# Kernel tuning notes

Measured on AMD Instinct MI355X. Metric: run time of the kernel, lower is better.

## Reference

```python
import jax, jax.numpy as jnp
import numpy as np

N = 2048      # factor dims (d_in == units == N)
K = 16        # nonzeros per row of each factor
B = 16384     # batch
F = 3         # number of sparse factors
NNZ = N * K


def _pattern(f):
    # Fixed, compile-time-known structured sparsity pattern (butterfly-like):
    # row r has nonzeros at cols (r + k*(N//K) + f) % N, k in [0, K)
    r = np.repeat(np.arange(N), K)
    k = np.tile(np.arange(K), N)
    c = (r + k * (N // K) + f) % N
    return r.astype(np.int32), c.astype(np.int32)


def setup_inputs() -> dict:
    key = jax.random.key(0)
    kx, k0, k1, k2, ks, kb = jax.random.split(key, 6)
    # glorot-ish scale for sparse factor values: fan ~ K nonzeros per row
    wscale = (2.0 / (K + K)) ** 0.5
    rows0, cols0 = _pattern(0)
    rows1, cols1 = _pattern(1)
    rows2, cols2 = _pattern(2)
    return {
        "x": jax.random.normal(kx, (B, N), dtype=jnp.float32),
        "vals0": jax.random.normal(k0, (NNZ,), dtype=jnp.float32) * wscale,
        "vals1": jax.random.normal(k1, (NNZ,), dtype=jnp.float32) * wscale,
        "vals2": jax.random.normal(k2, (NNZ,), dtype=jnp.float32) * wscale,
        "rows0": jnp.asarray(rows0), "cols0": jnp.asarray(cols0),
        "rows1": jnp.asarray(rows1), "cols1": jnp.asarray(cols1),
        "rows2": jnp.asarray(rows2), "cols2": jnp.asarray(cols2),
        "scaling": jax.random.uniform(ks, (1,), dtype=jnp.float32, minval=0.5, maxval=1.5),
        "bias": jax.random.normal(kb, (N,), dtype=jnp.float32) * 0.02,
    }


def _dense_factor(vals, rows, cols):
    # materialize the sparse factor (values scattered into the fixed pattern)
    return jnp.zeros((N, N), dtype=vals.dtype).at[rows, cols].set(vals)


def reference(x, vals0, vals1, vals2, rows0, cols0, rows1, cols1, rows2, cols2, scaling, bias):
    # output = relu(scaling * (x @ W0 @ W1 @ W2) + bias)
    y = x
    for vals, rows, cols in ((vals0, rows0, cols0), (vals1, rows1, cols1), (vals2, rows2, cols2)):
        y = y @ _dense_factor(vals, rows, cols)  # [B, N]
    y = scaling * y + bias
    return jax.nn.relu(y)
```

## Files before the change

### kernel.cpp

```cpp
#include <hip/hip_runtime.h>

#define NN 2048
#define KK 16

__global__ __launch_bounds__(256) void sfd_compose01(const float* __restrict__ v0,
                                                     const float* __restrict__ v1,
                                                     float* __restrict__ w01) {
  int tid = blockIdx.x * 256 + threadIdx.x;
  int c1 = tid >> 4;
  int i  = tid & 15;
  int cm = (c1 + NN - 1) & (NN - 1);
  int s1 = cm & 127;
  int t1 = cm >> 7;
  int rx = s1 + (i << 7);
  float acc = 0.f;
#pragma unroll
  for (int k1 = 0; k1 < 16; ++k1) {
    int r0 = (cm - (k1 << 7)) & (NN - 1);
    int k0 = (t1 - k1 - i) & 15;
    acc = fmaf(v1[r0 * 16 + k1], v0[rx * 16 + k0], acc);
  }
  w01[c1 * 16 + i] = acc;
}

__global__ __launch_bounds__(256) void sfd_compose012(const float* __restrict__ v2,
                                                      const float* __restrict__ w01,
                                                      const float* __restrict__ scaling,
                                                      float* __restrict__ mcl) {
  int tid = blockIdx.x * 256 + threadIdx.x;
  int c = tid >> 4;
  int i = tid & 15;
  float acc = 0.f;
#pragma unroll
  for (int k2 = 0; k2 < 16; ++k2) {
    int r1 = (c + NN - 2 - (k2 << 7)) & (NN - 1);
    acc = fmaf(v2[r1 * 16 + k2], w01[r1 * 16 + i], acc);
  }
  int s = c & 127;
  int j = c >> 7;
  mcl[(s * 16 + j) * 16 + i] = acc * scaling[0];
}

__global__ __launch_bounds__(256) void sfd_apply(const float* __restrict__ x,
                                                 const float* __restrict__ mcl,
                                                 const float* __restrict__ bias,
                                                 float* __restrict__ out) {
  const int S0 = blockIdx.x << 5;
  const int b0 = blockIdx.y << 6;
  const int t = threadIdx.x;
  const int s_idx = t & 31;
  const int jp = t >> 5;
  const int s = S0 + s_idx;
  const int j0 = jp << 1;

  float mc0[16], mc1[16];
  {
    const float4* p0 = (const float4*)(mcl + ((s * 16 + j0) << 4));
    const float4* p1 = (const float4*)(mcl + ((s * 16 + j0 + 1) << 4));
#pragma unroll
    for (int q = 0; q < 4; ++q) {
      float4 a = p0[q];
      mc0[4 * q + 0] = a.x; mc0[4 * q + 1] = a.y;
      mc0[4 * q + 2] = a.z; mc0[4 * q + 3] = a.w;
      float4 b = p1[q];
      mc1[4 * q + 0] = b.x; mc1[4 * q + 1] = b.y;
      mc1[4 * q + 2] = b.z; mc1[4 * q + 3] = b.w;
    }
  }
  const int c0 = s + (j0 << 7);
  const int c1 = c0 + 128;
  const float bi0 = bias[c0];
  const float bi1 = bias[c1];

  __shared__ float xs[8 * 512];

  for (int ch = 0; ch < 8; ++ch) {
    const int rb = b0 + (ch << 3);
#pragma unroll
    for (int q = 0; q < 16; ++q) {
      int idx = t + (q << 8);
      int u = idx & 31;
      int i = (idx >> 5) & 15;
      int r = idx >> 9;
      int col = ((S0 + 125 + u) & 127) + (i << 7);
      xs[idx] = x[(size_t)(rb + r) * NN + col];
    }
    __syncthreads();
#pragma unroll 1
    for (int r = 0; r < 8; ++r) {
      const float* xr = xs + (r << 9) + s_idx;
      float acc0 = 0.f, acc1 = 0.f;
#pragma unroll
      for (int i = 0; i < 16; ++i) {
        float xv = xr[i << 5];
        acc0 = fmaf(xv, mc0[i], acc0);
        acc1 = fmaf(xv, mc1[i], acc1);
      }
      size_t ob = (size_t)(rb + r) * NN;
      out[ob + c0] = fmaxf(acc0 + bi0, 0.f);
      out[ob + c1] = fmaxf(acc1 + bi1, 0.f);
    }
    __syncthreads();
  }
}

extern "C" void kernel_launch(void* const* d_in, const int* in_sizes, int n_in,
                              void* d_out, int out_size, void* d_ws, size_t ws_size,
                              hipStream_t stream) {
  const float* x       = (const float*)d_in[0];
  const float* v0      = (const float*)d_in[1];
  const float* v1      = (const float*)d_in[2];
  const float* v2      = (const float*)d_in[3];
  const float* scaling = (const float*)d_in[10];
  const float* bias    = (const float*)d_in[11];
  float* out = (float*)d_out;

  float* w01 = (float*)d_ws;
  float* mcl = w01 + NN * KK;

  const int B = in_sizes[0] / NN;

  hipLaunchKernelGGL(sfd_compose01, dim3(128), dim3(256), 0, stream, v0, v1, w01);
  hipLaunchKernelGGL(sfd_compose012, dim3(128), dim3(256), 0, stream, v2, w01, scaling, mcl);
  hipLaunchKernelGGL(sfd_apply, dim3(4, B >> 6), dim3(256), 0, stream, x, mcl, bias, out);
}
```

Baseline: 272.5 us.

## Re-layout shared x tile for float4 reads, halve batch per block, nontemporal stores

The apply kernel's shared-memory tile changes from an i-major layout to a per-(row,u) layout padded to 20 floats, so each thread reads its 16 x values with four float4 loads. To keep the math correct, the coefficients are rotated per thread by a wraparound shift. Each block now covers 32 batch rows instead of 64, which doubles the grid, and the launch bound requests 8 blocks per CU. Bias is folded into the accumulator init and outputs use nontemporal stores to avoid cache pollution. The cost is scalar global loads for coefficients and x gathers.

```diff
diff --git a/kernel.cpp b/kernel.cpp
--- a/kernel.cpp
+++ b/kernel.cpp
@@ -41,30 +41,28 @@
   mcl[(s * 16 + j) * 16 + i] = acc * scaling[0];
 }
 
-__global__ __launch_bounds__(256) void sfd_apply(const float* __restrict__ x,
-                                                 const float* __restrict__ mcl,
-                                                 const float* __restrict__ bias,
-                                                 float* __restrict__ out) {
+__global__ __launch_bounds__(256, 8) void sfd_apply(const float* __restrict__ x,
+                                                    const float* __restrict__ mcl,
+                                                    const float* __restrict__ bias,
+                                                    float* __restrict__ out) {
   const int S0 = blockIdx.x << 5;
-  const int b0 = blockIdx.y << 6;
+  const int b0 = blockIdx.y << 5;
   const int t = threadIdx.x;
-  const int s_idx = t & 31;
+  const int u = t & 31;
   const int jp = t >> 5;
-  const int s = S0 + s_idx;
+  const int s = S0 + u;
   const int j0 = jp << 1;
+  const int w0 = (S0 + 125) & 127;
+  const int shift = (w0 + u) >> 7;
 
   float mc0[16], mc1[16];
   {
-    const float4* p0 = (const float4*)(mcl + ((s * 16 + j0) << 4));
-    const float4* p1 = (const float4*)(mcl + ((s * 16 + j0 + 1) << 4));
+    const float* r0p = mcl + ((s * 16 + j0) << 4);
 #pragma unroll
-    for (int q = 0; q < 4; ++q) {
-      float4 a = p0[q];
-      mc0[4 * q + 0] = a.x; mc0[4 * q + 1] = a.y;
-      mc0[4 * q + 2] = a.z; mc0[4 * q + 3] = a.w;
-      float4 b = p1[q];
-      mc1[4 * q + 0] = b.x; mc1[4 * q + 1] = b.y;
-      mc1[4 * q + 2] = b.z; mc1[4 * q + 3] = b.w;
+    for (int i = 0; i < 16; ++i) {
+      int ic = (i + shift) & 15;
+      mc0[i] = r0p[ic];
+      mc1[i] = r0p[16 + ic];
     }
   }
   const int c0 = s + (j0 << 7);
@@ -72,33 +70,43 @@
   const float bi0 = bias[c0];
   const float bi1 = bias[c1];
 
-  __shared__ float xs[8 * 512];
+  __shared__ float xs[8 * 32 * 20];
 
-  for (int ch = 0; ch < 8; ++ch) {
+  for (int ch = 0; ch < 4; ++ch) {
     const int rb = b0 + (ch << 3);
 #pragma unroll
-    for (int q = 0; q < 16; ++q) {
+    for (int q = 0; q < 4; ++q) {
       int idx = t + (q << 8);
-      int u = idx & 31;
-      int i = (idx >> 5) & 15;
-      int r = idx >> 9;
-      int col = ((S0 + 125 + u) & 127) + (i << 7);
-      xs[idx] = x[(size_t)(rb + r) * NN + col];
+      int uu = idx & 31;
+      int ig = (idx >> 5) & 3;
+      int rr = idx >> 7;
+      const float* xrow = x + (size_t)(rb + rr) * NN;
+      int cb = w0 + uu + (ig << 9);
+      float4 v;
+      v.x = xrow[cb & (NN - 1)];
+      v.y = xrow[(cb + 128) & (NN - 1)];
+      v.z = xrow[(cb + 256) & (NN - 1)];
+      v.w = xrow[(cb + 384) & (NN - 1)];
+      *(float4*)(xs + (rr * 32 + uu) * 20 + (ig << 2)) = v;
     }
     __syncthreads();
 #pragma unroll 1
     for (int r = 0; r < 8; ++r) {
-      const float* xr = xs + (r << 9) + s_idx;
-      float acc0 = 0.f, acc1 = 0.f;
+      const float4* xr = (const float4*)(xs + (r * 32 + u) * 20);
+      float xv[16];
+      *(float4*)(xv + 0)  = xr[0];
+      *(float4*)(xv + 4)  = xr[1];
+      *(float4*)(xv + 8)  = xr[2];
+      *(float4*)(xv + 12) = xr[3];
+      float acc0 = bi0, acc1 = bi1;
 #pragma unroll
       for (int i = 0; i < 16; ++i) {
-        float xv = xr[i << 5];
-        acc0 = fmaf(xv, mc0[i], acc0);
-        acc1 = fmaf(xv, mc1[i], acc1);
+        acc0 = fmaf(xv[i], mc0[i], acc0);
+        acc1 = fmaf(xv[i], mc1[i], acc1);
       }
       size_t ob = (size_t)(rb + r) * NN;
-      out[ob + c0] = fmaxf(acc0 + bi0, 0.f);
-      out[ob + c1] = fmaxf(acc1 + bi1, 0.f);
+      __builtin_nontemporal_store(fmaxf(acc0, 0.f), &out[ob + c0]);
+      __builtin_nontemporal_store(fmaxf(acc1, 0.f), &out[ob + c1]);
     }
     __syncthreads();
   }
@@ -122,5 +130,5 @@
 
   hipLaunchKernelGGL(sfd_compose01, dim3(128), dim3(256), 0, stream, v0, v1, w01);
   hipLaunchKernelGGL(sfd_compose012, dim3(128), dim3(256), 0, stream, v2, w01, scaling, mcl);
-  hipLaunchKernelGGL(sfd_apply, dim3(4, B >> 6), dim3(256), 0, stream, x, mcl, bias, out);
+  hipLaunchKernelGGL(sfd_apply, dim3(4, B >> 5), dim3(256), 0, stream, x, mcl, bias, out);
 }
```

Result: no change. 272.5 us (-0.0%).
